# Performance work log

Measured on AMD Instinct MI355X. Metric: run time of the kernel, lower is better.

Reference implementation:

```python
import jax, jax.numpy as jnp
import numpy as np

B, S, D, H = 2, 2048, 1024, 16
HD = D // H


def setup_inputs() -> dict:
    key = jax.random.key(0)
    ks = jax.random.split(key, 6)
    std = 1.0 / np.sqrt(D)
    return {
        "hidden_states": jax.random.normal(ks[0], (B, S, D), dtype=jnp.float32),
        "attention_mask": jnp.zeros((B, 1, S, S), dtype=jnp.float32),
        "Wq": jax.random.normal(ks[1], (D, D), dtype=jnp.float32) * std,
        "bq": jnp.zeros((D,), dtype=jnp.float32),
        "Wk": jax.random.normal(ks[2], (D, D), dtype=jnp.float32) * std,
        "bk": jnp.zeros((D,), dtype=jnp.float32),
        "Wv": jax.random.normal(ks[3], (D, D), dtype=jnp.float32) * std,
        "bv": jnp.zeros((D,), dtype=jnp.float32),
        "Wo": jax.random.normal(ks[4], (D, D), dtype=jnp.float32) * std,
        "bo": jnp.zeros((D,), dtype=jnp.float32),
    }


def reference(hidden_states, attention_mask, Wq, bq, Wk, bk, Wv, bv, Wo, bo):
    scale = HD ** (-0.5)
    # torch Linear: y = x @ W^T + b
    def proj(x, W, b):
        y = jnp.einsum('bsd,ed->bse', x, W) + b
        return y.reshape(B, S, H, HD).transpose(0, 2, 1, 3)  # [B,H,S,HD]
    q = proj(hidden_states, Wq, bq)
    k = proj(hidden_states, Wk, bk)
    v = proj(hidden_states, Wv, bv)
    scores = jnp.einsum('bhqd,bhkd->bhqk', q, k) * scale + attention_mask
    attn = jax.nn.softmax(scores, axis=-1)  # dropout p=0.0 -> identity
    out = jnp.einsum('bhqk,bhkd->bhqd', attn, v)
    out = out.transpose(0, 2, 1, 3).reshape(B, S, D)
    return jnp.einsum('bsd,ed->bse', out, Wo) + bo
```

## Files before the change

### kernel.cpp

```cpp
#include <hip/hip_runtime.h>
#include <hip/hip_bf16.h>
#include <stdint.h>

#define Bb 2
#define Ss 2048
#define Dd 1024
#define Hh 16
#define HD 64

typedef __attribute__((ext_vector_type(8))) __bf16 bf16x8;
typedef __attribute__((ext_vector_type(4))) __bf16 bf16x4;
typedef __attribute__((ext_vector_type(4))) float f32x4;

#define LOG2E 1.44269504088896f

#define HS_N   (Bb * Ss * Dd)
#define W_N    (Dd * Dd)
#define B_N    (Dd)
#define CAN_HS 0
#define CAN_WQ (CAN_HS + HS_N)
#define CAN_BQ (CAN_WQ + W_N)
#define CAN_WK (CAN_BQ + B_N)
#define CAN_BK (CAN_WK + W_N)
#define CAN_WV (CAN_BK + B_N)
#define CAN_BV (CAN_WV + W_N)
#define CAN_WO (CAN_BV + B_N)
#define CAN_BO (CAN_WO + W_N)
#define CAN_END (CAN_BO + B_N)
#define TSZ    (Bb * Hh * Ss * HD)
#define WS_ELEMS (CAN_END + 4 * TSZ)
#define WS_NEED ((size_t)WS_ELEMS * 2)

__device__ __forceinline__ void gl_lds16(const __bf16* g, __bf16* l) {
  __builtin_amdgcn_global_load_lds(
      (const __attribute__((address_space(1))) void*)g,
      (__attribute__((address_space(3))) void*)l,
      16, 0, 0);
}

__global__ void canon_kernel(const float* hs, const float* Wq, const float* bq,
                             const float* Wk, const float* bk, const float* Wv,
                             const float* bv, const float* Wo, const float* bo,
                             __bf16* __restrict__ dst) {
  const float* srcs[9] = {hs, Wq, bq, Wk, bk, Wv, bv, Wo, bo};
  const long starts[10] = {CAN_HS, CAN_WQ, CAN_BQ, CAN_WK, CAN_BK,
                           CAN_WV, CAN_BV, CAN_WO, CAN_BO, CAN_END};
  const long nchunks = CAN_END / 8;
  for (long c = blockIdx.x * blockDim.x + threadIdx.x; c < nchunks;
       c += (long)gridDim.x * blockDim.x) {
    const long i = c * 8;
    int seg = 0;
#pragma unroll
    for (int t = 1; t < 9; t++) seg += (i >= starts[t]) ? 1 : 0;
    const float* s = srcs[seg] + (i - starts[seg]);
    bf16x8 v;
#pragma unroll
    for (int e = 0; e < 8; e++) v[e] = (__bf16)s[e];
    *(bf16x8*)(dst + i) = v;
  }
}

template <int MODE, typename OutT>
__global__ __launch_bounds__(256, 2) void gemm_bt(
    const __bf16* __restrict__ A,
    const __bf16* __restrict__ W0, const __bf16* __restrict__ W1,
    const __bf16* __restrict__ W2,
    const __bf16* __restrict__ b0, const __bf16* __restrict__ b1,
    const __bf16* __restrict__ b2,
    OutT* __restrict__ O0, OutT* __restrict__ O1, OutT* __restrict__ O2) {
  __shared__ __align__(16) __bf16 sA[128 * 32];
  __shared__ __align__(16) __bf16 sB[128 * 32];
  const int tid = threadIdx.x;
  const int lane = tid & 63;
  const int wid = tid >> 6;
  const int quad = lane >> 4;
  const int l15 = lane & 15;
  const int mBlock = blockIdx.x * 128;

  const __bf16* W;
  const __bf16* bias;
  OutT* Out;
  int nBlock, which = 0;
  if (MODE == 0) {
    which = blockIdx.y >> 3;
    nBlock = (blockIdx.y & 7) * 128;
    W = which == 0 ? W0 : (which == 1 ? W1 : W2);
    bias = which == 0 ? b0 : (which == 1 ? b1 : b2);
    Out = which == 0 ? O0 : (which == 1 ? O1 : O2);
  } else {
    nBlock = blockIdx.y * 128;
    W = W0;
    bias = b0;
    Out = O0;
  }

  const int waveM = (wid >> 1) * 64;
  const int waveN = (wid & 1) * 64;

  f32x4 acc[4][4] = {};

  const int c1 = wid * 64 + lane;
  const int c2 = c1 + 256;
  const __bf16* Ar1 = A + (mBlock + (c1 >> 2)) * Dd + (c1 & 3) * 8;
  const __bf16* Ar2 = A + (mBlock + (c2 >> 2)) * Dd + (c2 & 3) * 8;
  const __bf16* Wr1 = W + (nBlock + (c1 >> 2)) * Dd + (c1 & 3) * 8;
  const __bf16* Wr2 = W + (nBlock + (c2 >> 2)) * Dd + (c2 & 3) * 8;
  __bf16* ldsA1 = sA + (wid * 64) * 8;
  __bf16* ldsA2 = sA + (wid * 64 + 256) * 8;
  __bf16* ldsB1 = sB + (wid * 64) * 8;
  __bf16* ldsB2 = sB + (wid * 64 + 256) * 8;

  for (int k0 = 0; k0 < Dd; k0 += 32) {
    gl_lds16(Ar1 + k0, ldsA1);
    gl_lds16(Ar2 + k0, ldsA2);
    gl_lds16(Wr1 + k0, ldsB1);
    gl_lds16(Wr2 + k0, ldsB2);
    __syncthreads();

    bf16x8 aF[4], bF[4];
#pragma unroll
    for (int mi = 0; mi < 4; mi++)
      aF[mi] = *(const bf16x8*)(sA + (waveM + mi * 16 + l15) * 32 + quad * 8);
#pragma unroll
    for (int ni = 0; ni < 4; ni++)
      bF[ni] = *(const bf16x8*)(sB + (waveN + ni * 16 + l15) * 32 + quad * 8);
#pragma unroll
    for (int mi = 0; mi < 4; mi++)
#pragma unroll
      for (int ni = 0; ni < 4; ni++)
        acc[mi][ni] = __builtin_amdgcn_mfma_f32_16x16x32_bf16(
            aF[mi], bF[ni], acc[mi][ni], 0, 0, 0);
    __syncthreads();
  }

#pragma unroll
  for (int ni = 0; ni < 4; ni++) {
    const int ng = nBlock + waveN + ni * 16 + l15;
    const float bv = (float)bias[ng];
#pragma unroll
    for (int mi = 0; mi < 4; mi++) {
      const int mg0 = mBlock + waveM + mi * 16 + quad * 4;
#pragma unroll
      for (int r = 0; r < 4; r++) {
        const float v = acc[mi][ni][r] + bv;
        const int m = mg0 + r;
        if (MODE == 0) {
          const int b = m >> 11, s = m & 2047;
          const int h = ng >> 6, hd = ng & 63;
          if (which == 2)
            Out[(((b * Hh + h) * HD + hd) * Ss) + s] = (OutT)v;
          else
            Out[(((b * Hh + h) * Ss + s) * HD) + hd] = (OutT)v;
        } else {
          Out[m * Dd + ng] = (OutT)v;
        }
      }
    }
  }
}

__global__ __launch_bounds__(256, 4) void attn_fused(
    const __bf16* __restrict__ Qg, const __bf16* __restrict__ Kg,
    const __bf16* __restrict__ Vt, const float* __restrict__ Mf,
    __bf16* __restrict__ Og) {
  __shared__ __align__(16) __bf16 sK[2][64][32];
  __shared__ __align__(16) __bf16 sVt[2][64][32];
  __shared__ __align__(16) __bf16 sP[4][16][80];

  const int tid = threadIdx.x;
  const int lane = tid & 63;
  const int wid = tid >> 6;
  const int quad = lane >> 4;
  const int l15 = lane & 15;
  const int bh = blockIdx.y;
  const int b = bh >> 4;
  const int h = bh & 15;
  const int q0 = blockIdx.x * 64;
  const int q = q0 + wid * 16 + l15;

  const __bf16* Qp = Qg + (size_t)bh * Ss * HD;
  const __bf16* Kp = Kg + (size_t)bh * Ss * HD;
  const __bf16* Vp = Vt + (size_t)bh * HD * Ss;
  const float* Mrow = Mf + ((size_t)b * Ss + q) * Ss;

  bf16x8 qf[2];
#pragma unroll
  for (int ks = 0; ks < 2; ks++)
    qf[ks] = *(const bf16x8*)(Qp + (size_t)q * HD + ks * 32 + quad * 8);

  f32x4 o4[4] = {};
  float mrun = -1e30f;
  float lrun = 0.f;
  const float SCL2 = 0.125f * LOG2E;

  for (int kv0 = 0; kv0 < Ss; kv0 += 64) {
    f32x4 m4[4];
#pragma unroll
    for (int mi = 0; mi < 4; mi++)
      m4[mi] = *(const f32x4*)(Mrow + kv0 + mi * 16 + quad * 4);

#pragma unroll
    for (int j = 0; j < 2; j++) {
      const int c = j * 256 + tid;
      const int ks = c >> 8, rem = c & 255;
      const int row = rem >> 2, kc = c & 3;
      gl_lds16(Kp + (kv0 + row) * HD + ks * 32 + kc * 8, &sK[0][0][0] + c * 8);
    }
#pragma unroll
    for (int j = 0; j < 2; j++) {
      const int c = j * 256 + tid;
      const int ks = c >> 8, rem = c & 255;
      const int hd = rem >> 2, kc = c & 3;
      gl_lds16(Vp + (size_t)hd * Ss + kv0 + ks * 32 + kc * 8,
               &sVt[0][0][0] + c * 8);
    }
    __syncthreads();

    f32x4 s4[4] = {};
#pragma unroll
    for (int ks = 0; ks < 2; ks++) {
      bf16x8 kf[4];
#pragma unroll
      for (int mi = 0; mi < 4; mi++)
        kf[mi] = *(const bf16x8*)&sK[ks][mi * 16 + l15][quad * 8];
#pragma unroll
      for (int mi = 0; mi < 4; mi++)
        s4[mi] = __builtin_amdgcn_mfma_f32_16x16x32_bf16(kf[mi], qf[ks],
                                                         s4[mi], 0, 0, 0);
    }

#pragma unroll
    for (int mi = 0; mi < 4; mi++)
#pragma unroll
      for (int r = 0; r < 4; r++)
        s4[mi][r] = s4[mi][r] * SCL2 + m4[mi][r] * LOG2E;

    float vmax = -1e30f;
#pragma unroll
    for (int mi = 0; mi < 4; mi++)
#pragma unroll
      for (int r = 0; r < 4; r++) vmax = fmaxf(vmax, s4[mi][r]);
    vmax = fmaxf(vmax, __shfl_xor(vmax, 16));
    vmax = fmaxf(vmax, __shfl_xor(vmax, 32));

    const float mnew = fmaxf(mrun, vmax);
    const float alpha = exp2f(mrun - mnew);
    mrun = mnew;
    float rsum = 0.f;
#pragma unroll
    for (int mi = 0; mi < 4; mi++)
#pragma unroll
      for (int r = 0; r < 4; r++) {
        const float p = exp2f(s4[mi][r] - mnew);
        rsum += p;
        s4[mi][r] = p;
      }
    rsum += __shfl_xor(rsum, 16);
    rsum += __shfl_xor(rsum, 32);
    lrun = lrun * alpha + rsum;
#pragma unroll
    for (int mi = 0; mi < 4; mi++) o4[mi] *= alpha;

    asm volatile("s_waitcnt lgkmcnt(0)" ::: "memory");
#pragma unroll
    for (int mi = 0; mi < 4; mi++) {
      bf16x4 pk;
#pragma unroll
      for (int r = 0; r < 4; r++) pk[r] = (__bf16)s4[mi][r];
      *(bf16x4*)&sP[wid][l15][mi * 16 + quad * 4] = pk;
    }
    asm volatile("s_waitcnt lgkmcnt(0)" ::: "memory");

#pragma unroll
    for (int ks = 0; ks < 2; ks++) {
      bf16x8 pf = *(const bf16x8*)&sP[wid][l15][ks * 32 + quad * 8];
      bf16x8 vf[4];
#pragma unroll
      for (int mi = 0; mi < 4; mi++)
        vf[mi] = *(const bf16x8*)&sVt[ks][mi * 16 + l15][quad * 8];
#pragma unroll
      for (int mi = 0; mi < 4; mi++)
        o4[mi] = __builtin_amdgcn_mfma_f32_16x16x32_bf16(vf[mi], pf, o4[mi],
                                                         0, 0, 0);
    }
    __syncthreads();
  }

  const float inv = 1.0f / lrun;
  __bf16* Ow = Og + (((size_t)b * Ss + q) * Hh + h) * HD;
#pragma unroll
  for (int mi = 0; mi < 4; mi++) {
    bf16x4 pk;
#pragma unroll
    for (int r = 0; r < 4; r++) pk[r] = (__bf16)(o4[mi][r] * inv);
    *(bf16x4*)(Ow + mi * 16 + quad * 4) = pk;
  }
}

extern "C" void kernel_launch(void* const* d_in, const int* in_sizes, int n_in,
                              void* d_out, int out_size, void* d_ws,
                              size_t ws_size, hipStream_t stream) {
  if (ws_size < WS_NEED) return;

  __bf16* ws = (__bf16*)d_ws;
  const __bf16* hsC = ws + CAN_HS;
  const __bf16* WqC = ws + CAN_WQ;
  const __bf16* bqC = ws + CAN_BQ;
  const __bf16* WkC = ws + CAN_WK;
  const __bf16* bkC = ws + CAN_BK;
  const __bf16* WvC = ws + CAN_WV;
  const __bf16* bvC = ws + CAN_BV;
  const __bf16* WoC = ws + CAN_WO;
  const __bf16* boC = ws + CAN_BO;
  __bf16* Q = ws + CAN_END;
  __bf16* K = Q + TSZ;
  __bf16* V = K + TSZ;
  __bf16* AW = V + TSZ;
  float* out = (float*)d_out;

  canon_kernel<<<2048, 256, 0, stream>>>(
      (const float*)d_in[0], (const float*)d_in[2], (const float*)d_in[3],
      (const float*)d_in[4], (const float*)d_in[5], (const float*)d_in[6],
      (const float*)d_in[7], (const float*)d_in[8], (const float*)d_in[9], ws);
  gemm_bt<0, __bf16><<<dim3(32, 24), 256, 0, stream>>>(
      hsC, WqC, WkC, WvC, bqC, bkC, bvC, Q, K, V);
  attn_fused<<<dim3(32, 32), 256, 0, stream>>>(Q, K, V, (const float*)d_in[1],
                                               AW);
  gemm_bt<1, float><<<dim3(32, 8), 256, 0, stream>>>(
      AW, WoC, WoC, WoC, boC, boC, boC, out, out, out);
}
```

Measured before the change: 276.8 us.

## Double attention KV tile to 128 keys and vectorize transposed V store

The attention kernel now processes 128 keys per iteration instead of 64. This halves the number of barriers and online-softmax rescale steps per query block, but raises register and LDS use, so the occupancy hint drops from 4 to 3 blocks. Separately, the V projection epilogue packs four consecutive sequence elements into one bf16x4 store instead of four strided scalar stores. Larger per-iteration state may increase register pressure or spills.

After: 278.3 us. Within noise of the previous version (+0.5%).

```diff
diff --git a/kernel.cpp b/kernel.cpp
--- a/kernel.cpp
+++ b/kernel.cpp
@@ -140,32 +140,38 @@
 #pragma unroll
     for (int mi = 0; mi < 4; mi++) {
       const int mg0 = mBlock + waveM + mi * 16 + quad * 4;
-#pragma unroll
-      for (int r = 0; r < 4; r++) {
-        const float v = acc[mi][ni][r] + bv;
-        const int m = mg0 + r;
-        if (MODE == 0) {
-          const int b = m >> 11, s = m & 2047;
-          const int h = ng >> 6, hd = ng & 63;
-          if (which == 2)
-            Out[(((b * Hh + h) * HD + hd) * Ss) + s] = (OutT)v;
-          else
+      if (MODE == 0 && which == 2) {
+        const int b = mg0 >> 11, s0 = mg0 & 2047;
+        const int h = ng >> 6, hd = ng & 63;
+        bf16x4 pk;
+#pragma unroll
+        for (int r = 0; r < 4; r++) pk[r] = (__bf16)(acc[mi][ni][r] + bv);
+        *(bf16x4*)((__bf16*)Out + (((b * Hh + h) * HD + hd) * Ss) + s0) = pk;
+      } else {
+#pragma unroll
+        for (int r = 0; r < 4; r++) {
+          const float v = acc[mi][ni][r] + bv;
+          const int m = mg0 + r;
+          if (MODE == 0) {
+            const int b = m >> 11, s = m & 2047;
+            const int h = ng >> 6, hd = ng & 63;
             Out[(((b * Hh + h) * Ss + s) * HD) + hd] = (OutT)v;
-        } else {
-          Out[m * Dd + ng] = (OutT)v;
+          } else {
+            Out[m * Dd + ng] = (OutT)v;
+          }
         }
       }
     }
   }
 }
 
-__global__ __launch_bounds__(256, 4) void attn_fused(
+__global__ __launch_bounds__(256, 3) void attn_fused(
     const __bf16* __restrict__ Qg, const __bf16* __restrict__ Kg,
     const __bf16* __restrict__ Vt, const float* __restrict__ Mf,
     __bf16* __restrict__ Og) {
-  __shared__ __align__(16) __bf16 sK[2][64][32];
-  __shared__ __align__(16) __bf16 sVt[2][64][32];
-  __shared__ __align__(16) __bf16 sP[4][16][80];
+  __shared__ __align__(16) __bf16 sK[2][128][32];
+  __shared__ __align__(16) __bf16 sVt[4][64][32];
+  __shared__ __align__(16) __bf16 sP[4][16][136];
 
   const int tid = threadIdx.x;
   const int lane = tid & 63;
@@ -193,21 +199,21 @@
   float lrun = 0.f;
   const float SCL2 = 0.125f * LOG2E;
 
-  for (int kv0 = 0; kv0 < Ss; kv0 += 64) {
-    f32x4 m4[4];
-#pragma unroll
-    for (int mi = 0; mi < 4; mi++)
+  for (int kv0 = 0; kv0 < Ss; kv0 += 128) {
+    f32x4 m4[8];
+#pragma unroll
+    for (int mi = 0; mi < 8; mi++)
       m4[mi] = *(const f32x4*)(Mrow + kv0 + mi * 16 + quad * 4);
 
 #pragma unroll
-    for (int j = 0; j < 2; j++) {
+    for (int j = 0; j < 4; j++) {
       const int c = j * 256 + tid;
-      const int ks = c >> 8, rem = c & 255;
+      const int ks = c >> 9, rem = c & 511;
       const int row = rem >> 2, kc = c & 3;
       gl_lds16(Kp + (kv0 + row) * HD + ks * 32 + kc * 8, &sK[0][0][0] + c * 8);
     }
 #pragma unroll
-    for (int j = 0; j < 2; j++) {
+    for (int j = 0; j < 4; j++) {
       const int c = j * 256 + tid;
       const int ks = c >> 8, rem = c & 255;
       const int hd = rem >> 2, kc = c & 3;
@@ -216,28 +222,25 @@
     }
     __syncthreads();
 
-    f32x4 s4[4] = {};
-#pragma unroll
-    for (int ks = 0; ks < 2; ks++) {
-      bf16x8 kf[4];
-#pragma unroll
-      for (int mi = 0; mi < 4; mi++)
-        kf[mi] = *(const bf16x8*)&sK[ks][mi * 16 + l15][quad * 8];
-#pragma unroll
-      for (int mi = 0; mi < 4; mi++)
-        s4[mi] = __builtin_amdgcn_mfma_f32_16x16x32_bf16(kf[mi], qf[ks],
-                                                         s4[mi], 0, 0, 0);
-    }
-
-#pragma unroll
-    for (int mi = 0; mi < 4; mi++)
+    f32x4 s4[8] = {};
+#pragma unroll
+    for (int ks = 0; ks < 2; ks++)
+#pragma unroll
+      for (int mi = 0; mi < 8; mi++) {
+        bf16x8 kf = *(const bf16x8*)&sK[ks][mi * 16 + l15][quad * 8];
+        s4[mi] = __builtin_amdgcn_mfma_f32_16x16x32_bf16(kf, qf[ks], s4[mi],
+                                                         0, 0, 0);
+      }
+
+#pragma unroll
+    for (int mi = 0; mi < 8; mi++)
 #pragma unroll
       for (int r = 0; r < 4; r++)
         s4[mi][r] = s4[mi][r] * SCL2 + m4[mi][r] * LOG2E;
 
     float vmax = -1e30f;
 #pragma unroll
-    for (int mi = 0; mi < 4; mi++)
+    for (int mi = 0; mi < 8; mi++)
 #pragma unroll
       for (int r = 0; r < 4; r++) vmax = fmaxf(vmax, s4[mi][r]);
     vmax = fmaxf(vmax, __shfl_xor(vmax, 16));
@@ -248,7 +251,7 @@
     mrun = mnew;
     float rsum = 0.f;
 #pragma unroll
-    for (int mi = 0; mi < 4; mi++)
+    for (int mi = 0; mi < 8; mi++)
 #pragma unroll
       for (int r = 0; r < 4; r++) {
         const float p = exp2f(s4[mi][r] - mnew);
@@ -263,7 +266,7 @@
 
     asm volatile("s_waitcnt lgkmcnt(0)" ::: "memory");
 #pragma unroll
-    for (int mi = 0; mi < 4; mi++) {
+    for (int mi = 0; mi < 8; mi++) {
       bf16x4 pk;
 #pragma unroll
       for (int r = 0; r < 4; r++) pk[r] = (__bf16)s4[mi][r];
@@ -272,16 +275,14 @@
     asm volatile("s_waitcnt lgkmcnt(0)" ::: "memory");
 
 #pragma unroll
-    for (int ks = 0; ks < 2; ks++) {
+    for (int ks = 0; ks < 4; ks++) {
       bf16x8 pf = *(const bf16x8*)&sP[wid][l15][ks * 32 + quad * 8];
-      bf16x8 vf[4];
-#pragma unroll
-      for (int mi = 0; mi < 4; mi++)
-        vf[mi] = *(const bf16x8*)&sVt[ks][mi * 16 + l15][quad * 8];
-#pragma unroll
-      for (int mi = 0; mi < 4; mi++)
-        o4[mi] = __builtin_amdgcn_mfma_f32_16x16x32_bf16(vf[mi], pf, o4[mi],
+#pragma unroll
+      for (int mi = 0; mi < 4; mi++) {
+        bf16x8 vf = *(const bf16x8*)&sVt[ks][mi * 16 + l15][quad * 8];
+        o4[mi] = __builtin_amdgcn_mfma_f32_16x16x32_bf16(vf, pf, o4[mi],
                                                          0, 0, 0);
+      }
     }
     __syncthreads();
   }
```
